# Optimization experiments

Measured on AMD Instinct MI355X. Metric: run time of the kernel, lower is better.

## Reference

```python
import jax, jax.numpy as jnp
import numpy as np

B, L = 8, 896
D_MODEL, N_HEAD, D_HEAD, D_INNER = 320, 10, 32, 1280
LN_EPS = 1e-5


def layernorm(x, g, b):
    mu = jnp.mean(x, axis=-1, keepdims=True)
    var = jnp.mean(jnp.square(x - mu), axis=-1, keepdims=True)
    return (x - mu) * jax.lax.rsqrt(var + LN_EPS) * g + b


def setup_inputs() -> dict:
    key = jax.random.key(0)
    ks = jax.random.split(key, 8)
    w = lambda k, shape: (jax.random.normal(k, shape, jnp.float32) * 0.02)
    return {
        "Z": jax.random.normal(ks[0], (B, L, D_MODEL), jnp.float32),
        "D": jax.random.uniform(ks[1], (B, L, L), jnp.float32),  # nonneg sq-distance bias
        "new_mask": jnp.zeros((B, L, L), jnp.float32),           # additive mask (0 = keep)
        "mask": jnp.ones((B, L, L), jnp.float32),                # multiplicative validity mask
        "gamma": jnp.ones((4, 4), jnp.float32),
        "w_qkv": w(ks[2], (D_MODEL, 3 * D_MODEL)),
        "b_qkv": jnp.zeros((3 * D_MODEL,), jnp.float32),
        "w_o": w(ks[3], (D_MODEL, D_MODEL)),
        "ln1_g": jnp.ones((D_MODEL,), jnp.float32),
        "ln1_b": jnp.zeros((D_MODEL,), jnp.float32),
        "ln2_g": jnp.ones((D_MODEL,), jnp.float32),
        "ln2_b": jnp.zeros((D_MODEL,), jnp.float32),
        "w1": w(ks[4], (D_MODEL, D_INNER)),
        "b1": jnp.zeros((D_INNER,), jnp.float32),
        "w2": w(ks[5], (D_INNER, D_MODEL)),
        "b2": jnp.zeros((D_MODEL,), jnp.float32),
        "N": 128, "M": 256, "P": 512,
    }


def reference(Z, D, new_mask, mask, gamma, w_qkv, b_qkv, w_o,
              ln1_g, ln1_b, ln2_g, ln2_b, w1, b1, w2, b2, N, M, P):
    bsz, n_elem, _ = Z.shape
    sqrtd = np.sqrt(D_HEAD).astype(np.float32)

    # per-pair type bias: segment ids 0=atom,1=bond,2=triplet (use_quad=False)
    seg = jnp.concatenate([
        jnp.zeros((N,), jnp.int32),
        jnp.ones((M,), jnp.int32),
        jnp.full((P,), 2, jnp.int32),
    ])  # [L]
    gamma_mask = gamma[seg[:, None], seg[None, :]]  # [L, L]

    inp = Z
    Zn = layernorm(Z, ln1_g, ln1_b)
    qkv = (Zn @ w_qkv + b_qkv).reshape(bsz, n_elem, N_HEAD, 3 * D_HEAD)
    Z2, Z3, Z4 = jnp.split(qkv, 3, axis=3)  # each [b, L, h, d]

    # scores [b, h, n, m]
    scores = jnp.einsum('bnhd,bmhd->bhnm', Z3, Z4) / sqrtd
    W = -(gamma_mask[None] * D)[:, None] + scores + new_mask[:, None]
    W = jax.nn.softmax(W, axis=3) * mask[:, None]

    attn_out = jnp.einsum('bhnm,bmhd->bnhd', W, Z2).reshape(bsz, n_elem, D_MODEL)
    attn_out = jax.nn.leaky_relu(attn_out, 0.01) @ w_o  # o_net has no bias
    Z_res = attn_out + inp

    Zn2 = layernorm(Z_res, ln2_g, ln2_b)
    out = jax.nn.relu(Zn2 @ w1 + b1) @ w2 + b2 + Z_res
    return out
```

## Files before the change

### kernel.cpp

```cpp
#include <hip/hip_runtime.h>

#define BB 8
#define LLEN 896
#define DMODEL 320
#define NHEAD 10
#define DHEAD 32
#define DINNER 1280
#define ROWS (BB*LLEN)

typedef float f32x4 __attribute__((ext_vector_type(4)));
typedef float f32x16 __attribute__((ext_vector_type(16)));
typedef __bf16 bf16x8 __attribute__((ext_vector_type(8)));
typedef short s16x8 __attribute__((ext_vector_type(8)));

__device__ __forceinline__ float bf2f(unsigned short u) {
    union { unsigned int i; float f; } x;
    x.i = ((unsigned int)u) << 16;
    return x.f;
}
__device__ __forceinline__ unsigned short f2bf(float f) {
    unsigned int u = __float_as_uint(f);
    u += 0x7FFF + ((u >> 16) & 1);
    return (unsigned short)(u >> 16);
}

__global__ __launch_bounds__(256) void transpose_bf16(const float* __restrict__ src,
                                                      unsigned short* __restrict__ dst,
                                                      int R, int C) {
    __shared__ float tile[32][33];
    int c0 = blockIdx.x * 32;
    int r0 = blockIdx.y * 32;
    int tx = threadIdx.x & 31, ty = threadIdx.x >> 5;
#pragma unroll
    for (int k = 0; k < 4; ++k) {
        int yy = ty + 8 * k;
        tile[yy][tx] = src[(size_t)(r0 + yy) * C + c0 + tx];
    }
    __syncthreads();
#pragma unroll
    for (int k = 0; k < 4; ++k) {
        int yy = ty + 8 * k;
        dst[(size_t)(c0 + yy) * R + r0 + tx] = f2bf(tile[tx][yy]);
    }
}

__global__ __launch_bounds__(256) void prepass(const float* __restrict__ D,
                                               const float* __restrict__ nm,
                                               const float* __restrict__ mk,
                                               const float* __restrict__ gamma,
                                               unsigned int* __restrict__ combo) {
    __shared__ unsigned int tile[32][33];
    int m0 = blockIdx.x * 32;
    int n0 = blockIdx.y * 32;
    int b = blockIdx.z;
    int sn = (n0 < 128) ? 0 : (n0 < 384) ? 1 : 2;
    int sm = (m0 < 128) ? 0 : (m0 < 384) ? 1 : 2;
    float g = gamma[sn * 4 + sm];
    int tx = threadIdx.x & 31, ty = threadIdx.x >> 5;
#pragma unroll
    for (int k = 0; k < 4; ++k) {
        int nl = ty + 8 * k;
        size_t idx = ((size_t)b * LLEN + n0 + nl) * LLEN + m0 + tx;
        float bias = -g * D[idx] + nm[idx];
        tile[nl][tx] = (unsigned int)f2bf(bias) | ((unsigned int)f2bf(mk[idx]) << 16);
    }
    __syncthreads();
#pragma unroll
    for (int k = 0; k < 4; ++k) {
        int ml = ty + 8 * k;
        combo[((size_t)b * LLEN + m0 + ml) * LLEN + n0 + tx] = tile[tx][ml];
    }
}

__global__ __launch_bounds__(320) void ln_kernel(const float* __restrict__ x,
                                                 const float* __restrict__ g,
                                                 const float* __restrict__ bia,
                                                 unsigned short* __restrict__ y) {
    int row = blockIdx.x;
    int t = threadIdx.x;
    float v = x[(size_t)row * DMODEL + t];
    float s = v;
#pragma unroll
    for (int o = 1; o < 64; o <<= 1) s += __shfl_xor(s, o, 64);
    __shared__ float red[10];
    int w = t >> 6;
    if ((t & 63) == 0) red[w] = s;
    __syncthreads();
    float mu = (red[0] + red[1] + red[2] + red[3] + red[4]) * (1.0f / DMODEL);
    float d = v - mu;
    float s2 = d * d;
#pragma unroll
    for (int o = 1; o < 64; o <<= 1) s2 += __shfl_xor(s2, o, 64);
    if ((t & 63) == 0) red[5 + w] = s2;
    __syncthreads();
    float var = (red[5] + red[6] + red[7] + red[8] + red[9]) * (1.0f / DMODEL);
    float inv = rsqrtf(var + 1e-5f);
    y[(size_t)row * DMODEL + t] = f2bf(d * inv * g[t] + bia[t]);
}

template <int EPI>
__global__ __launch_bounds__(256) void gemm_bt(const unsigned short* __restrict__ A,
                                               const unsigned short* __restrict__ BT,
                                               const float* __restrict__ bias,
                                               const float* __restrict__ resid,
                                               void* __restrict__ outv,
                                               int M, int N, int K) {
    __shared__ unsigned short As[64][40];
    __shared__ unsigned short Bs[64][40];
    int tid = threadIdx.x;
    int m0 = blockIdx.x * 64;
    int n0 = blockIdx.y * 64;
    int wid = tid >> 6, l = tid & 63;
    int wr = wid >> 1, wc = wid & 1;
    int sr = tid >> 2, sc = (tid & 3) * 8;
    int lr = l & 15, lh = l >> 4;
    f32x4 acc00 = {0.f, 0.f, 0.f, 0.f}, acc01 = acc00, acc10 = acc00, acc11 = acc00;

    for (int k0 = 0; k0 < K; k0 += 32) {
        __syncthreads();
        *(int4*)&As[sr][sc] = *(const int4*)&A[(size_t)(m0 + sr) * K + k0 + sc];
        *(int4*)&Bs[sr][sc] = *(const int4*)&BT[(size_t)(n0 + sr) * K + k0 + sc];
        __syncthreads();
        bf16x8 a0 = *(const bf16x8*)&As[wr * 32 + lr][lh * 8];
        bf16x8 a1 = *(const bf16x8*)&As[wr * 32 + 16 + lr][lh * 8];
        bf16x8 b0 = *(const bf16x8*)&Bs[wc * 32 + lr][lh * 8];
        bf16x8 b1 = *(const bf16x8*)&Bs[wc * 32 + 16 + lr][lh * 8];
        acc00 = __builtin_amdgcn_mfma_f32_16x16x32_bf16(a0, b0, acc00, 0, 0, 0);
        acc01 = __builtin_amdgcn_mfma_f32_16x16x32_bf16(a0, b1, acc01, 0, 0, 0);
        acc10 = __builtin_amdgcn_mfma_f32_16x16x32_bf16(a1, b0, acc10, 0, 0, 0);
        acc11 = __builtin_amdgcn_mfma_f32_16x16x32_bf16(a1, b1, acc11, 0, 0, 0);
    }

    unsigned short* outb = (unsigned short*)outv;
    float* outf = (float*)outv;
#pragma unroll
    for (int mi = 0; mi < 2; ++mi)
#pragma unroll
        for (int ni = 0; ni < 2; ++ni) {
            f32x4 a = (mi == 0) ? ((ni == 0) ? acc00 : acc01) : ((ni == 0) ? acc10 : acc11);
            int col = n0 + wc * 32 + ni * 16 + lr;
#pragma unroll
            for (int j = 0; j < 4; ++j) {
                int row = m0 + wr * 32 + mi * 16 + lh * 4 + j;
                float v = a[j];
                if (EPI == 0 || EPI == 2 || EPI == 3) v += bias[col];
                if (EPI == 2) v = fmaxf(v, 0.0f);
                if (EPI == 1 || EPI == 3) v += resid[(size_t)row * N + col];
                if (EPI == 0 || EPI == 2) outb[(size_t)row * N + col] = f2bf(v);
                else outf[(size_t)row * N + col] = v;
            }
        }
}

__global__ __launch_bounds__(640) void attn_mfma(const unsigned short* __restrict__ qkv,
                                                 const unsigned int* __restrict__ combo,
                                                 unsigned short* __restrict__ attn) {
    int tid = threadIdx.x;
    int h = tid >> 6;
    int l = tid & 63;
    int c = l & 31;
    int hi = l >> 5;
    int nt = blockIdx.x % 28;
    int b = blockIdx.x / 28;
    int n0 = nt * 32;

    size_t qbase = ((size_t)(b * LLEN + n0 + c)) * 960 + h * 96 + 32 + hi * 8;
    bf16x8 qB0 = *(const bf16x8*)&qkv[qbase];
    bf16x8 qB1 = *(const bf16x8*)&qkv[qbase + 16];

    f32x16 oacc = {0.f,0.f,0.f,0.f,0.f,0.f,0.f,0.f,0.f,0.f,0.f,0.f,0.f,0.f,0.f,0.f};
    float lsum = 0.f;

    const unsigned int* crow = combo + (size_t)b * LLEN * LLEN + n0 + c;
    size_t kbase = (size_t)b * LLEN * 960 + h * 96 + 64 + hi * 8;
    size_t vbase = (size_t)b * LLEN * 960 + h * 96 + c;

    for (int mt = 0; mt < 28; ++mt) {
        size_t krow = kbase + (size_t)(mt * 32 + c) * 960;
        bf16x8 kA0 = *(const bf16x8*)&qkv[krow];
        bf16x8 kA1 = *(const bf16x8*)&qkv[krow + 16];
        f32x16 sacc = {0.f,0.f,0.f,0.f,0.f,0.f,0.f,0.f,0.f,0.f,0.f,0.f,0.f,0.f,0.f,0.f};
        sacc = __builtin_amdgcn_mfma_f32_32x32x16_bf16(kA0, qB0, sacc, 0, 0, 0);
        sacc = __builtin_amdgcn_mfma_f32_32x32x16_bf16(kA1, qB1, sacc, 0, 0, 0);

        float p[16];
#pragma unroll
        for (int r = 0; r < 16; ++r) {
            int m = mt * 32 + (r & 3) + 8 * (r >> 2) + 4 * hi;
            unsigned int cm = crow[(size_t)m * LLEN];
            float bias = bf2f((unsigned short)(cm & 0xffffu));
            float mk = bf2f((unsigned short)(cm >> 16));
            float s = fmaf(sacc[r], 0.17677669529663687f, bias);
            float e = __expf(s);
            lsum += e;
            p[r] = e * mk;
        }

        unsigned int u[8], x[8];
#pragma unroll
        for (int j = 0; j < 8; ++j) {
            u[j] = (unsigned int)f2bf(p[2 * j]) | ((unsigned int)f2bf(p[2 * j + 1]) << 16);
            x[j] = (unsigned int)__shfl_xor((int)u[j], 32, 64);
        }
        union { unsigned int w[4]; bf16x8 v; } a1, a2;
        if (hi == 0) {
            a1.w[0] = u[0]; a1.w[1] = u[1]; a1.w[2] = x[0]; a1.w[3] = x[1];
            a2.w[0] = u[4]; a2.w[1] = u[5]; a2.w[2] = x[4]; a2.w[3] = x[5];
        } else {
            a1.w[0] = x[2]; a1.w[1] = x[3]; a1.w[2] = u[2]; a1.w[3] = u[3];
            a2.w[0] = x[6]; a2.w[1] = x[7]; a2.w[2] = u[6]; a2.w[3] = u[7];
        }

        union { unsigned short s[8]; bf16x8 v; } v1, v2;
#pragma unroll
        for (int e = 0; e < 8; ++e) {
            v1.s[e] = qkv[vbase + (size_t)(mt * 32 + hi * 8 + e) * 960];
            v2.s[e] = qkv[vbase + (size_t)(mt * 32 + 16 + hi * 8 + e) * 960];
        }
        oacc = __builtin_amdgcn_mfma_f32_32x32x16_bf16(a1.v, v1.v, oacc, 0, 0, 0);
        oacc = __builtin_amdgcn_mfma_f32_32x32x16_bf16(a2.v, v2.v, oacc, 0, 0, 0);
    }

    lsum += __shfl_xor(lsum, 32, 64);
    __shared__ float ls[NHEAD][32];
    ls[h][c] = 1.0f / lsum;
    __syncthreads();
#pragma unroll
    for (int r = 0; r < 16; ++r) {
        int n = (r & 3) + 8 * (r >> 2) + 4 * hi;
        float o = oacc[r] * ls[h][n];
        o = (o >= 0.f) ? o : 0.01f * o;
        attn[((size_t)(b * LLEN + n0 + n)) * DMODEL + h * DHEAD + c] = f2bf(o);
    }
}

extern "C" void kernel_launch(void* const* d_in, const int* in_sizes, int n_in,
                              void* d_out, int out_size, void* d_ws, size_t ws_size,
                              hipStream_t stream) {
    const float* Z     = (const float*)d_in[0];
    const float* Dm    = (const float*)d_in[1];
    const float* nmask = (const float*)d_in[2];
    const float* mask  = (const float*)d_in[3];
    const float* gamma = (const float*)d_in[4];
    const float* w_qkv = (const float*)d_in[5];
    const float* b_qkv = (const float*)d_in[6];
    const float* w_o   = (const float*)d_in[7];
    const float* ln1g  = (const float*)d_in[8];
    const float* ln1b  = (const float*)d_in[9];
    const float* ln2g  = (const float*)d_in[10];
    const float* ln2b  = (const float*)d_in[11];
    const float* w1    = (const float*)d_in[12];
    const float* b1    = (const float*)d_in[13];
    const float* w2    = (const float*)d_in[14];
    const float* b2    = (const float*)d_in[15];

    char* ws = (char*)d_ws;
    unsigned short* Zn    = (unsigned short*)(ws + 0);
    unsigned short* qkv   = (unsigned short*)(ws + 4587520);
    unsigned short* attn  = (unsigned short*)(ws + 18350080);
    float*          Zres  = (float*)(ws + 22937600);
    unsigned short* Zn2   = (unsigned short*)(ws + 32112640);
    unsigned short* Hbuf  = (unsigned short*)(ws + 36700160);
    unsigned short* wqkvT = (unsigned short*)(ws + 55050240);
    unsigned short* woT   = (unsigned short*)(ws + 55664640);
    unsigned short* w1T   = (unsigned short*)(ws + 55869440);
    unsigned short* w2T   = (unsigned short*)(ws + 56688640);
    unsigned int*   combo = (unsigned int*)(ws + 57507840);

    transpose_bf16<<<dim3(960 / 32, 320 / 32), 256, 0, stream>>>(w_qkv, wqkvT, 320, 960);
    transpose_bf16<<<dim3(320 / 32, 320 / 32), 256, 0, stream>>>(w_o, woT, 320, 320);
    transpose_bf16<<<dim3(1280 / 32, 320 / 32), 256, 0, stream>>>(w1, w1T, 320, 1280);
    transpose_bf16<<<dim3(320 / 32, 1280 / 32), 256, 0, stream>>>(w2, w2T, 1280, 320);

    prepass<<<dim3(28, 28, 8), 256, 0, stream>>>(Dm, nmask, mask, gamma, combo);

    ln_kernel<<<ROWS, 320, 0, stream>>>(Z, ln1g, ln1b, Zn);

    gemm_bt<0><<<dim3(ROWS / 64, 960 / 64), 256, 0, stream>>>(Zn, wqkvT, b_qkv, nullptr,
                                                              (void*)qkv, ROWS, 960, 320);

    attn_mfma<<<BB * 28, 640, 0, stream>>>(qkv, combo, attn);

    gemm_bt<1><<<dim3(ROWS / 64, 320 / 64), 256, 0, stream>>>(attn, woT, nullptr, Z,
                                                              (void*)Zres, ROWS, 320, 320);

    ln_kernel<<<ROWS, 320, 0, stream>>>(Zres, ln2g, ln2b, Zn2);

    gemm_bt<2><<<dim3(ROWS / 64, 1280 / 64), 256, 0, stream>>>(Zn2, w1T, b1, nullptr,
                                                               (void*)Hbuf, ROWS, 1280, 320);

    gemm_bt<3><<<dim3(ROWS / 64, 320 / 64), 256, 0, stream>>>(Hbuf, w2T, b2, Zres,
                                                              d_out, ROWS, 320, 1280);
}
```

Before: 300.2 us.

## Retile GEMMs with direct-to-LDS loads, relayout bias/mask and V for attention

The GEMM moves to 128x64 tiles with a K step of 64, filled through global_load_lds 16-byte loads, and each wave now runs eight MFMA accumulators. The combined bias/mask buffer is rewritten in a tiled [b][mt][n][32] layout so attention can read it with vector int4 loads. A new kernel transposes V so each attention lane loads 8 contiguous bf16 values instead of 16 strided scalar gathers. Attention is split across two blocks of five heads, and the LDS normalization pass plus its barrier are replaced by a shuffle. The cost is an extra launch and an extra V buffer, and the unpadded 128-byte LDS rows may cause bank conflicts on MFMA operand reads.

```diff
diff --git a/kernel.cpp b/kernel.cpp
--- a/kernel.cpp
+++ b/kernel.cpp
@@ -24,6 +24,12 @@
     return (unsigned short)(u >> 16);
 }
 
+#define GLOAD16(g, l)                                                              \
+    __builtin_amdgcn_global_load_lds(                                              \
+        (const __attribute__((address_space(1))) void*)(g),                        \
+        (__attribute__((address_space(3))) void*)(__attribute__((address_space(3))) char*)(l), \
+        16, 0, 0)
+
 __global__ __launch_bounds__(256) void transpose_bf16(const float* __restrict__ src,
                                                       unsigned short* __restrict__ dst,
                                                       int R, int C) {
@@ -50,7 +56,7 @@
                                                const float* __restrict__ gamma,
                                                unsigned int* __restrict__ combo) {
     __shared__ unsigned int tile[32][33];
-    int m0 = blockIdx.x * 32;
+    int mt = blockIdx.x, m0 = mt * 32;
     int n0 = blockIdx.y * 32;
     int b = blockIdx.z;
     int sn = (n0 < 128) ? 0 : (n0 < 384) ? 1 : 2;
@@ -67,8 +73,26 @@
     __syncthreads();
 #pragma unroll
     for (int k = 0; k < 4; ++k) {
+        int nl = ty + 8 * k;
+        combo[(((size_t)b * 28 + mt) * LLEN + n0 + nl) * 32 + tx] = tile[nl][tx];
+    }
+}
+
+__global__ __launch_bounds__(256) void vt_kernel(const unsigned short* __restrict__ qkv,
+                                                 unsigned short* __restrict__ Vt) {
+    __shared__ unsigned short tile[32][33];
+    int mt = blockIdx.x, h = blockIdx.y, b = blockIdx.z;
+    int tx = threadIdx.x & 31, ty = threadIdx.x >> 5;
+#pragma unroll
+    for (int k = 0; k < 4; ++k) {
         int ml = ty + 8 * k;
-        combo[((size_t)b * LLEN + m0 + ml) * LLEN + n0 + tx] = tile[tx][ml];
+        tile[ml][tx] = qkv[((size_t)(b * LLEN) + mt * 32 + ml) * 960 + h * 96 + tx];
+    }
+    __syncthreads();
+#pragma unroll
+    for (int k = 0; k < 4; ++k) {
+        int d = ty + 8 * k;
+        Vt[(((size_t)b * NHEAD + h) * 32 + d) * LLEN + mt * 32 + tx] = tile[tx][d];
     }
 }
 
@@ -105,45 +129,61 @@
                                                const float* __restrict__ resid,
                                                void* __restrict__ outv,
                                                int M, int N, int K) {
-    __shared__ unsigned short As[64][40];
-    __shared__ unsigned short Bs[64][40];
+    __shared__ unsigned short As[128][64];
+    __shared__ unsigned short Bs[64][64];
     int tid = threadIdx.x;
-    int m0 = blockIdx.x * 64;
+    int m0 = blockIdx.x * 128;
     int n0 = blockIdx.y * 64;
     int wid = tid >> 6, l = tid & 63;
     int wr = wid >> 1, wc = wid & 1;
-    int sr = tid >> 2, sc = (tid & 3) * 8;
     int lr = l & 15, lh = l >> 4;
-    f32x4 acc00 = {0.f, 0.f, 0.f, 0.f}, acc01 = acc00, acc10 = acc00, acc11 = acc00;
-
-    for (int k0 = 0; k0 < K; k0 += 32) {
+    int srow = tid >> 3;
+    int scol = (tid & 7) * 8;
+    int wlds = (tid >> 6) * 1024;
+
+    f32x4 acc[4][2];
+#pragma unroll
+    for (int mi = 0; mi < 4; ++mi)
+#pragma unroll
+        for (int ni = 0; ni < 2; ++ni) acc[mi][ni] = (f32x4){0.f, 0.f, 0.f, 0.f};
+
+    for (int k0 = 0; k0 < K; k0 += 64) {
         __syncthreads();
-        *(int4*)&As[sr][sc] = *(const int4*)&A[(size_t)(m0 + sr) * K + k0 + sc];
-        *(int4*)&Bs[sr][sc] = *(const int4*)&BT[(size_t)(n0 + sr) * K + k0 + sc];
+#pragma unroll
+        for (int i = 0; i < 4; ++i)
+            GLOAD16(&A[(size_t)(m0 + i * 32 + srow) * K + k0 + scol],
+                    (char*)&As[0][0] + i * 4096 + wlds);
+#pragma unroll
+        for (int i = 0; i < 2; ++i)
+            GLOAD16(&BT[(size_t)(n0 + i * 32 + srow) * K + k0 + scol],
+                    (char*)&Bs[0][0] + i * 4096 + wlds);
         __syncthreads();
-        bf16x8 a0 = *(const bf16x8*)&As[wr * 32 + lr][lh * 8];
-        bf16x8 a1 = *(const bf16x8*)&As[wr * 32 + 16 + lr][lh * 8];
-        bf16x8 b0 = *(const bf16x8*)&Bs[wc * 32 + lr][lh * 8];
-        bf16x8 b1 = *(const bf16x8*)&Bs[wc * 32 + 16 + lr][lh * 8];
-        acc00 = __builtin_amdgcn_mfma_f32_16x16x32_bf16(a0, b0, acc00, 0, 0, 0);
-        acc01 = __builtin_amdgcn_mfma_f32_16x16x32_bf16(a0, b1, acc01, 0, 0, 0);
-        acc10 = __builtin_amdgcn_mfma_f32_16x16x32_bf16(a1, b0, acc10, 0, 0, 0);
-        acc11 = __builtin_amdgcn_mfma_f32_16x16x32_bf16(a1, b1, acc11, 0, 0, 0);
+#pragma unroll
+        for (int kk = 0; kk < 2; ++kk) {
+            bf16x8 b0 = *(const bf16x8*)&Bs[wc * 32 + lr][kk * 32 + lh * 8];
+            bf16x8 b1 = *(const bf16x8*)&Bs[wc * 32 + 16 + lr][kk * 32 + lh * 8];
+#pragma unroll
+            for (int mi = 0; mi < 4; ++mi) {
+                bf16x8 a = *(const bf16x8*)&As[wr * 64 + mi * 16 + lr][kk * 32 + lh * 8];
+                acc[mi][0] = __builtin_amdgcn_mfma_f32_16x16x32_bf16(a, b0, acc[mi][0], 0, 0, 0);
+                acc[mi][1] = __builtin_amdgcn_mfma_f32_16x16x32_bf16(a, b1, acc[mi][1], 0, 0, 0);
+            }
+        }
     }
 
     unsigned short* outb = (unsigned short*)outv;
     float* outf = (float*)outv;
 #pragma unroll
-    for (int mi = 0; mi < 2; ++mi)
+    for (int mi = 0; mi < 4; ++mi)
 #pragma unroll
         for (int ni = 0; ni < 2; ++ni) {
-            f32x4 a = (mi == 0) ? ((ni == 0) ? acc00 : acc01) : ((ni == 0) ? acc10 : acc11);
             int col = n0 + wc * 32 + ni * 16 + lr;
+            float bv = (EPI != 1) ? bias[col] : 0.f;
 #pragma unroll
             for (int j = 0; j < 4; ++j) {
-                int row = m0 + wr * 32 + mi * 16 + lh * 4 + j;
-                float v = a[j];
-                if (EPI == 0 || EPI == 2 || EPI == 3) v += bias[col];
+                int row = m0 + wr * 64 + mi * 16 + lh * 4 + j;
+                float v = acc[mi][ni][j];
+                if (EPI == 0 || EPI == 2 || EPI == 3) v += bv;
                 if (EPI == 2) v = fmaxf(v, 0.0f);
                 if (EPI == 1 || EPI == 3) v += resid[(size_t)row * N + col];
                 if (EPI == 0 || EPI == 2) outb[(size_t)row * N + col] = f2bf(v);
@@ -152,11 +192,12 @@
         }
 }
 
-__global__ __launch_bounds__(640) void attn_mfma(const unsigned short* __restrict__ qkv,
+__global__ __launch_bounds__(320) void attn_mfma(const unsigned short* __restrict__ qkv,
+                                                 const unsigned short* __restrict__ Vt,
                                                  const unsigned int* __restrict__ combo,
                                                  unsigned short* __restrict__ attn) {
     int tid = threadIdx.x;
-    int h = tid >> 6;
+    int h = blockIdx.y * 5 + (tid >> 6);
     int l = tid & 63;
     int c = l & 31;
     int hi = l >> 5;
@@ -171,9 +212,9 @@
     f32x16 oacc = {0.f,0.f,0.f,0.f,0.f,0.f,0.f,0.f,0.f,0.f,0.f,0.f,0.f,0.f,0.f,0.f};
     float lsum = 0.f;
 
-    const unsigned int* crow = combo + (size_t)b * LLEN * LLEN + n0 + c;
+    const unsigned int* cbase = combo + ((size_t)b * 28 * LLEN + n0 + c) * 32;
     size_t kbase = (size_t)b * LLEN * 960 + h * 96 + 64 + hi * 8;
-    size_t vbase = (size_t)b * LLEN * 960 + h * 96 + c;
+    const unsigned short* vrow = Vt + (((size_t)b * NHEAD + h) * 32 + c) * LLEN;
 
     for (int mt = 0; mt < 28; ++mt) {
         size_t krow = kbase + (size_t)(mt * 32 + c) * 960;
@@ -183,11 +224,15 @@
         sacc = __builtin_amdgcn_mfma_f32_32x32x16_bf16(kA0, qB0, sacc, 0, 0, 0);
         sacc = __builtin_amdgcn_mfma_f32_32x32x16_bf16(kA1, qB1, sacc, 0, 0, 0);
 
+        const unsigned int* cp = cbase + (size_t)mt * (LLEN * 32);
+        int4 x4[4];
+#pragma unroll
+        for (int g = 0; g < 4; ++g) x4[g] = *(const int4*)&cp[8 * g + 4 * hi];
+
         float p[16];
 #pragma unroll
         for (int r = 0; r < 16; ++r) {
-            int m = mt * 32 + (r & 3) + 8 * (r >> 2) + 4 * hi;
-            unsigned int cm = crow[(size_t)m * LLEN];
+            unsigned int cm = ((const unsigned int*)x4)[(r >> 2) * 4 + (r & 3)];
             float bias = bf2f((unsigned short)(cm & 0xffffu));
             float mk = bf2f((unsigned short)(cm >> 16));
             float s = fmaf(sacc[r], 0.17677669529663687f, bias);
@@ -199,7 +244,10 @@
         unsigned int u[8], x[8];
 #pragma unroll
         for (int j = 0; j < 8; ++j) {
-            u[j] = (unsigned int)f2bf(p[2 * j]) | ((unsigned int)f2bf(p[2 * j + 1]) << 16);
+            union { __bf16 h2[2]; unsigned int w; } pk;
+            pk.h2[0] = (__bf16)p[2 * j];
+            pk.h2[1] = (__bf16)p[2 * j + 1];
+            u[j] = pk.w;
             x[j] = (unsigned int)__shfl_xor((int)u[j], 32, 64);
         }
         union { unsigned int w[4]; bf16x8 v; } a1, a2;
@@ -211,24 +259,18 @@
             a2.w[0] = x[6]; a2.w[1] = x[7]; a2.w[2] = u[6]; a2.w[3] = u[7];
         }
 
-        union { unsigned short s[8]; bf16x8 v; } v1, v2;
-#pragma unroll
-        for (int e = 0; e < 8; ++e) {
-            v1.s[e] = qkv[vbase + (size_t)(mt * 32 + hi * 8 + e) * 960];
-            v2.s[e] = qkv[vbase + (size_t)(mt * 32 + 16 + hi * 8 + e) * 960];
-        }
-        oacc = __builtin_amdgcn_mfma_f32_32x32x16_bf16(a1.v, v1.v, oacc, 0, 0, 0);
-        oacc = __builtin_amdgcn_mfma_f32_32x32x16_bf16(a2.v, v2.v, oacc, 0, 0, 0);
+        bf16x8 v1 = *(const bf16x8*)&vrow[mt * 32 + hi * 8];
+        bf16x8 v2 = *(const bf16x8*)&vrow[mt * 32 + 16 + hi * 8];
+        oacc = __builtin_amdgcn_mfma_f32_32x32x16_bf16(a1.v, v1, oacc, 0, 0, 0);
+        oacc = __builtin_amdgcn_mfma_f32_32x32x16_bf16(a2.v, v2, oacc, 0, 0, 0);
     }
 
     lsum += __shfl_xor(lsum, 32, 64);
-    __shared__ float ls[NHEAD][32];
-    ls[h][c] = 1.0f / lsum;
-    __syncthreads();
+    float invs = 1.0f / lsum;
 #pragma unroll
     for (int r = 0; r < 16; ++r) {
         int n = (r & 3) + 8 * (r >> 2) + 4 * hi;
-        float o = oacc[r] * ls[h][n];
+        float o = oacc[r] * __shfl(invs, n, 64);
         o = (o >= 0.f) ? o : 0.01f * o;
         attn[((size_t)(b * LLEN + n0 + n)) * DMODEL + h * DHEAD + c] = f2bf(o);
     }
@@ -266,6 +308,7 @@
     unsigned short* w1T   = (unsigned short*)(ws + 55869440);
     unsigned short* w2T   = (unsigned short*)(ws + 56688640);
     unsigned int*   combo = (unsigned int*)(ws + 57507840);
+    unsigned short* Vtb   = (unsigned short*)(ws + 83197952);
 
     transpose_bf16<<<dim3(960 / 32, 320 / 32), 256, 0, stream>>>(w_qkv, wqkvT, 320, 960);
     transpose_bf16<<<dim3(320 / 32, 320 / 32), 256, 0, stream>>>(w_o, woT, 320, 320);
@@ -276,19 +319,21 @@
 
     ln_kernel<<<ROWS, 320, 0, stream>>>(Z, ln1g, ln1b, Zn);
 
-    gemm_bt<0><<<dim3(ROWS / 64, 960 / 64), 256, 0, stream>>>(Zn, wqkvT, b_qkv, nullptr,
-                                                              (void*)qkv, ROWS, 960, 320);
-
-    attn_mfma<<<BB * 28, 640, 0, stream>>>(qkv, combo, attn);
-
-    gemm_bt<1><<<dim3(ROWS / 64, 320 / 64), 256, 0, stream>>>(attn, woT, nullptr, Z,
-                                                              (void*)Zres, ROWS, 320, 320);
+    gemm_bt<0><<<dim3(ROWS / 128, 960 / 64), 256, 0, stream>>>(Zn, wqkvT, b_qkv, nullptr,
+                                                               (void*)qkv, ROWS, 960, 320);
+
+    vt_kernel<<<dim3(28, NHEAD, BB), 256, 0, stream>>>(qkv, Vtb);
+
+    attn_mfma<<<dim3(BB * 28, 2), 320, 0, stream>>>(qkv, Vtb, combo, attn);
+
+    gemm_bt<1><<<dim3(ROWS / 128, 320 / 64), 256, 0, stream>>>(attn, woT, nullptr, Z,
+                                                               (void*)Zres, ROWS, 320, 320);
 
     ln_kernel<<<ROWS, 320, 0, stream>>>(Zres, ln2g, ln2b, Zn2);
 
-    gemm_bt<2><<<dim3(ROWS / 64, 1280 / 64), 256, 0, stream>>>(Zn2, w1T, b1, nullptr,
-                                                               (void*)Hbuf, ROWS, 1280, 320);
-
-    gemm_bt<3><<<dim3(ROWS / 64, 320 / 64), 256, 0, stream>>>(Hbuf, w2T, b2, Zres,
-                                                              d_out, ROWS, 320, 1280);
-}
+    gemm_bt<2><<<dim3(ROWS / 128, 1280 / 64), 256, 0, stream>>>(Zn2, w1T, b1, nullptr,
+                                                                (void*)Hbuf, ROWS, 1280, 320);
+
+    gemm_bt<3><<<dim3(ROWS / 128, 320 / 64), 256, 0, stream>>>(Hbuf, w2T, b2, Zres,
+                                                               d_out, ROWS, 320, 1280);
+}
```

After: 308.6 us. 2.8% more time.
